# Kernel optimization log

Hardware: AMD Instinct MI355X
Metric: run time of the kernel (lower is better)

## Reference

```python
import jax, jax.numpy as jnp
import numpy as np

N_NODES = 100000
IN_F = 512
HID = 256
HEADS = 1
CLASSES = 40
ALPHA = 0.5
EPS = 1e-5


def layer_norm(x, g, b):
    mu = jnp.mean(x, axis=-1, keepdims=True)
    var = jnp.mean(jnp.square(x - mu), axis=-1, keepdims=True)
    return g * (x - mu) / jnp.sqrt(var + EPS) + b


def full_attention_conv(qs, ks, vs):
    # qs, ks, vs: [N, H, D]; global (Frobenius) L2 normalization as in torch.norm(p=2)
    qs = qs / jnp.linalg.norm(qs.reshape(-1))
    ks = ks / jnp.linalg.norm(ks.reshape(-1))
    N = qs.shape[0]
    kvs = jnp.einsum('lhm,lhd->hmd', ks, vs)                  # [H, D, D]
    attention_num = jnp.einsum('nhm,hmd->nhd', qs, kvs) + N * vs
    ks_sum = jnp.sum(ks, axis=0)                              # [H, D]
    attention_normalizer = jnp.einsum('nhm,hm->nh', qs, ks_sum)[..., None] + N
    return attention_num / attention_normalizer               # [N, H, D]


def trans_layer(h, prev, Wq, bq, Wk, bk, Wv, bv, ln_g, ln_b):
    N = h.shape[0]
    q = (h @ Wq + bq).reshape(N, HEADS, HID)
    k = (h @ Wk + bk).reshape(N, HEADS, HID)
    v = (h @ Wv + bv).reshape(N, HEADS, HID)
    attn = full_attention_conv(q, k, v).mean(axis=1)          # [N, HID]
    h = ALPHA * attn + (1.0 - ALPHA) * prev
    return layer_norm(h, ln_g, ln_b)


def setup_inputs() -> dict:
    key = jax.random.key(0)
    ks = jax.random.split(key, 16)
    s_in = 1.0 / np.sqrt(IN_F)
    s_h = 1.0 / np.sqrt(HID)
    d = {
        'x': jax.random.normal(ks[0], (N_NODES, IN_F), jnp.float32),
        'edge_index': jax.random.randint(ks[1], (2, 1600000), 0, N_NODES, jnp.int64),
        'W_in': jax.random.normal(ks[2], (IN_F, HID), jnp.float32) * s_in,
        'b_in': jnp.zeros((HID,), jnp.float32),
        'ln0_g': jnp.ones((HID,), jnp.float32),
        'ln0_b': jnp.zeros((HID,), jnp.float32),
        'Wq0': jax.random.normal(ks[3], (HID, HID * HEADS), jnp.float32) * s_h,
        'bq0': jnp.zeros((HID * HEADS,), jnp.float32),
        'Wk0': jax.random.normal(ks[4], (HID, HID * HEADS), jnp.float32) * s_h,
        'bk0': jnp.zeros((HID * HEADS,), jnp.float32),
        'Wv0': jax.random.normal(ks[5], (HID, HID * HEADS), jnp.float32) * s_h,
        'bv0': jnp.zeros((HID * HEADS,), jnp.float32),
        'ln1_g': jnp.ones((HID,), jnp.float32),
        'ln1_b': jnp.zeros((HID,), jnp.float32),
        'Wq1': jax.random.normal(ks[6], (HID, HID * HEADS), jnp.float32) * s_h,
        'bq1': jnp.zeros((HID * HEADS,), jnp.float32),
        'Wk1': jax.random.normal(ks[7], (HID, HID * HEADS), jnp.float32) * s_h,
        'bk1': jnp.zeros((HID * HEADS,), jnp.float32),
        'Wv1': jax.random.normal(ks[8], (HID, HID * HEADS), jnp.float32) * s_h,
        'bv1': jnp.zeros((HID * HEADS,), jnp.float32),
        'ln2_g': jnp.ones((HID,), jnp.float32),
        'ln2_b': jnp.zeros((HID,), jnp.float32),
        'W_out': jax.random.normal(ks[9], (HID, CLASSES), jnp.float32) * s_h,
        'b_out': jnp.zeros((CLASSES,), jnp.float32),
    }
    return d


def reference(x, edge_index, W_in, b_in, ln0_g, ln0_b,
              Wq0, bq0, Wk0, bk0, Wv0, bv0, ln1_g, ln1_b,
              Wq1, bq1, Wk1, bk1, Wv1, bv1, ln2_g, ln2_b,
              W_out, b_out):
    # SGFormer forward with use_graph=False, eval mode (dropout no-op).
    h = jax.nn.relu(layer_norm(x @ W_in + b_in, ln0_g, ln0_b))
    prev = h
    h = trans_layer(h, prev, Wq0, bq0, Wk0, bk0, Wv0, bv0, ln1_g, ln1_b)
    prev = h
    h = trans_layer(h, prev, Wq1, bq1, Wk1, bk1, Wv1, bv1, ln2_g, ln2_b)
    return h @ W_out + b_out  # [N, CLASSES]
```

## Files before the change

kernel.cpp:

```cpp
#include <hip/hip_runtime.h>


typedef __attribute__((ext_vector_type(8))) short short8;
typedef __attribute__((ext_vector_type(4))) float floatx4;

__device__ __forceinline__ float bf2f(short u) {
    union { unsigned int i; float f; } v;
    v.i = ((unsigned int)(unsigned short)u) << 16;
    return v.f;
}
__device__ __forceinline__ short f2bf(float f) {
    union { float f; unsigned int i; } v; v.f = f;
    unsigned int b = v.i + 0x7fffu + ((v.i >> 16) & 1u);
    return (short)(b >> 16);
}

#define HID 256
#define MROWS 100000
#define EPSLN 1e-5f

__device__ __forceinline__ void stage_a256(const short* __restrict__ A, short* As,
                                           int row0, int wave, int lane)
{
    const int base = wave * 512;
#pragma unroll
    for (int it = 0; it < 8; ++it) {
        int J = base + it * 64 + lane;
        int row = J >> 5, jj = J & 31;
        int c = jj ^ (row & 31);
        int rowg = min(row0 + row, MROWS - 1);
        const short* gp = A + (size_t)rowg * HID + c * 8;
        __builtin_amdgcn_global_load_lds(
            (const __attribute__((address_space(1))) void*)gp,
            (__attribute__((address_space(3))) void*)&As[(size_t)(base + it * 64) * 8],
            16, 0, 0);
    }
}
__device__ __forceinline__ void stage_lin256(const short* __restrict__ A, short* As,
                                             int row0, int wave, int lane)
{
    const int base = wave * 512;
#pragma unroll
    for (int it = 0; it < 8; ++it) {
        int J = base + it * 64 + lane;
        int row = J >> 5, jj = J & 31;
        int rowg = min(row0 + row, MROWS - 1);
        const short* gp = A + (size_t)rowg * HID + jj * 8;
        __builtin_amdgcn_global_load_lds(
            (const __attribute__((address_space(1))) void*)gp,
            (__attribute__((address_space(3))) void*)&As[(size_t)(base + it * 64) * 8],
            16, 0, 0);
    }
}
__device__ __forceinline__ short8 read_a256(const short* As, int m, int ki, int quad, int l15)
{
    int row = m * 16 + l15;
    int phys = (ki * 4 + quad) ^ (row & 31);
    return *(const short8*)&As[((size_t)row * 32 + phys) * 8];
}

__global__ __launch_bounds__(256, 3)
void qkv_kernel(const short* __restrict__ h,
                const short* __restrict__ BTq, const short* __restrict__ BTk,
                const short* __restrict__ BTv,
                const float* __restrict__ bq, const float* __restrict__ bk,
                const float* __restrict__ bv,
                short* __restrict__ qO, short* __restrict__ kO, short* __restrict__ vO,
                float* __restrict__ sqq, float* __restrict__ sqk,
                float* __restrict__ ksum)
{
    __shared__ short As[64 * 256];
    __shared__ short Cb[16 * 264];
    __shared__ float scr;

    const int tid = threadIdx.x, wave = tid >> 6, lane = tid & 63;
    const int quad = lane >> 4, l15 = lane & 15;
    const int row0 = blockIdx.x * 64, nb = wave * 64;

    stage_a256(h, As, row0, wave, lane);
    __syncthreads();

    const short* BTs[3] = {BTq, BTk, BTv};
    short* Cs[3] = {qO, kO, vO};
    const float* bs[3] = {bq, bk, bv};

#pragma unroll
    for (int out = 0; out < 3; ++out) {
        const short* BT = BTs[out];
        short* C = Cs[out];
        const float* bias = bs[out];

        floatx4 acc[4][4];
#pragma unroll
        for (int m = 0; m < 4; m++)
#pragma unroll
            for (int n = 0; n < 4; n++) acc[m][n] = (floatx4)0.0f;

#pragma unroll
        for (int ki = 0; ki < 8; ++ki) {
            short8 a[4];
#pragma unroll
            for (int m = 0; m < 4; ++m) a[m] = read_a256(As, m, ki, quad, l15);
#pragma unroll
            for (int n = 0; n < 4; ++n) {
                short8 b = *(const short8*)(BT + (size_t)(nb + n * 16 + l15) * 256 + ki * 32 + quad * 8);
#pragma unroll
                for (int m = 0; m < 4; ++m)
                    acc[m][n] = __builtin_amdgcn_mfma_f32_16x16x32_bf16(a[m], b, acc[m][n], 0, 0, 0);
            }
        }

        float bn[4];
#pragma unroll
        for (int n = 0; n < 4; n++) bn[n] = bias[nb + n * 16 + l15];

        float ssq = 0.f;
        float csum[4] = {0.f, 0.f, 0.f, 0.f};
#pragma unroll
        for (int m = 0; m < 4; m++)
#pragma unroll
            for (int r = 0; r < 4; r++) {
                int rl = m * 16 + quad * 4 + r;
                bool valid = (row0 + rl) < MROWS;
#pragma unroll
                for (int n = 0; n < 4; n++) {
                    float val = acc[m][n][r] + bn[n];
                    acc[m][n][r] = val;
                    if (valid) {
                        if (out < 2) ssq += val * val;
                        if (out == 1) csum[n] += val;
                    }
                }
            }
        if (out < 2) {
#pragma unroll
            for (int off = 32; off; off >>= 1) ssq += __shfl_down(ssq, off);
            if (tid == 0) scr = 0.f;
            __syncthreads();
            if (lane == 0) atomicAdd(&scr, ssq);
            __syncthreads();
            if (tid == 0) atomicAdd(out == 0 ? sqq : sqk, scr);
        }
        if (out == 1) {
#pragma unroll
            for (int n = 0; n < 4; n++) {
                float cv = csum[n];
                cv += __shfl_xor(cv, 16);
                cv += __shfl_xor(cv, 32);
                if (quad == 0) atomicAdd(&ksum[nb + n * 16 + l15], cv);
            }
        }
#pragma unroll
        for (int m = 0; m < 4; ++m) {
            __syncthreads();
#pragma unroll
            for (int n = 0; n < 4; ++n)
#pragma unroll
                for (int r = 0; r < 4; ++r)
                    Cb[(quad * 4 + r) * 264 + nb + n * 16 + l15] = f2bf(acc[m][n][r]);
            __syncthreads();
#pragma unroll
            for (int ch = tid; ch < 512; ch += 256) {
                int rl = ch >> 5, co = (ch & 31) * 8;
                int row = row0 + m * 16 + rl;
                if (row < MROWS)
                    *(short8*)(C + (size_t)row * 256 + co) = *(const short8*)&Cb[rl * 264 + co];
            }
        }
    }
}

__global__ __launch_bounds__(256, 3)
void attn_kernel(const short* __restrict__ q, const short* __restrict__ KVt,
                 const short* __restrict__ v, short* __restrict__ h,
                 const float* __restrict__ lng, const float* __restrict__ lnb,
                 float Nf)
{
    __shared__ short As[64 * 256];
    __shared__ short Cb[16 * 264];
    __shared__ float redS[64][4], redQ[64][4];
    __shared__ float rowm[64], rowr[64], denA[64];

    const int tid = threadIdx.x, wave = tid >> 6, lane = tid & 63;
    const int quad = lane >> 4, l15 = lane & 15;
    const int row0 = blockIdx.x * 64, nb = wave * 64;

    stage_a256(q, As, row0, wave, lane);
    __syncthreads();

    floatx4 acc[4][4];
#pragma unroll
    for (int m = 0; m < 4; m++)
#pragma unroll
        for (int n = 0; n < 4; n++) acc[m][n] = (floatx4)0.0f;
    floatx4 accd[4];
#pragma unroll
    for (int m = 0; m < 4; m++) accd[m] = (floatx4)0.0f;

#pragma unroll
    for (int ki = 0; ki < 8; ++ki) {
        short8 a[4];
#pragma unroll
        for (int m = 0; m < 4; ++m) a[m] = read_a256(As, m, ki, quad, l15);
#pragma unroll
        for (int n = 0; n < 4; ++n) {
            short8 b = *(const short8*)(KVt + (size_t)(nb + n * 16 + l15) * 256 + ki * 32 + quad * 8);
#pragma unroll
            for (int m = 0; m < 4; ++m)
                acc[m][n] = __builtin_amdgcn_mfma_f32_16x16x32_bf16(a[m], b, acc[m][n], 0, 0, 0);
        }
        if (wave == 0) {
            short8 bd = *(const short8*)(KVt + (size_t)(256 + l15) * 256 + ki * 32 + quad * 8);
#pragma unroll
            for (int m = 0; m < 4; ++m)
                accd[m] = __builtin_amdgcn_mfma_f32_16x16x32_bf16(a[m], bd, accd[m], 0, 0, 0);
        }
    }
    if (wave == 0 && l15 == 0) {
#pragma unroll
        for (int m = 0; m < 4; m++)
#pragma unroll
            for (int r = 0; r < 4; r++)
                denA[m * 16 + quad * 4 + r] = accd[m][r];
    }
    __syncthreads();

    stage_lin256(v, As, row0, wave, lane);
    __syncthreads();
#pragma unroll
    for (int m = 0; m < 4; m++)
#pragma unroll
        for (int r = 0; r < 4; r++) {
            int rl = m * 16 + quad * 4 + r;
            float rden = 1.0f / (denA[rl] + Nf);
#pragma unroll
            for (int n = 0; n < 4; n++) {
                int col = nb + n * 16 + l15;
                float vv = bf2f(As[(size_t)rl * 256 + col]);
                acc[m][n][r] = 0.5f * (acc[m][n][r] + Nf * vv) * rden;
            }
        }
    __syncthreads();

    stage_lin256(h, As, row0, wave, lane);
    __syncthreads();
#pragma unroll
    for (int m = 0; m < 4; m++)
#pragma unroll
        for (int r = 0; r < 4; r++) {
            int rl = m * 16 + quad * 4 + r;
            float s = 0.f, s2 = 0.f;
#pragma unroll
            for (int n = 0; n < 4; n++) {
                int col = nb + n * 16 + l15;
                float pv = bf2f(As[(size_t)rl * 256 + col]);
                float val = acc[m][n][r] + 0.5f * pv;
                acc[m][n][r] = val;
                s += val; s2 += val * val;
            }
#pragma unroll
            for (int off = 1; off < 16; off <<= 1) {
                s += __shfl_xor(s, off);
                s2 += __shfl_xor(s2, off);
            }
            if (l15 == 0) { redS[rl][wave] = s; redQ[rl][wave] = s2; }
        }
    __syncthreads();
    if (tid < 64) {
        float s = redS[tid][0] + redS[tid][1] + redS[tid][2] + redS[tid][3];
        float s2 = redQ[tid][0] + redQ[tid][1] + redQ[tid][2] + redQ[tid][3];
        float mean = s * (1.0f / 256.0f);
        float var = s2 * (1.0f / 256.0f) - mean * mean;
        rowm[tid] = mean;
        rowr[tid] = rsqrtf(var + EPSLN);
    }
    __syncthreads();
    float g[4], bb[4];
#pragma unroll
    for (int n = 0; n < 4; n++) {
        g[n] = lng[nb + n * 16 + l15];
        bb[n] = lnb[nb + n * 16 + l15];
    }
#pragma unroll
    for (int m = 0; m < 4; ++m) {
        __syncthreads();
#pragma unroll
        for (int n = 0; n < 4; ++n)
#pragma unroll
            for (int r = 0; r < 4; ++r) {
                int rl = m * 16 + quad * 4 + r;
                float x = (acc[m][n][r] - rowm[rl]) * rowr[rl] * g[n] + bb[n];
                Cb[(quad * 4 + r) * 264 + nb + n * 16 + l15] = f2bf(x);
            }
        __syncthreads();
#pragma unroll
        for (int ch = tid; ch < 512; ch += 256) {
            int rl = ch >> 5, co = (ch & 31) * 8;
            int row = row0 + m * 16 + rl;
            if (row < MROWS)
                *(short8*)(h + (size_t)row * 256 + co) = *(const short8*)&Cb[rl * 264 + co];
        }
    }
}

__global__ __launch_bounds__(256, 3)
void in_kernel(const float* __restrict__ x, const short* __restrict__ WinT,
               const float* __restrict__ b_in, const float* __restrict__ lng,
               const float* __restrict__ lnb, short* __restrict__ h)
{
    __shared__ short As[2][64 * 128];
    __shared__ short Cb[16 * 264];
    __shared__ float redS[64][4], redQ[64][4];
    __shared__ float rowm[64], rowr[64];

    const int tid = threadIdx.x, wave = tid >> 6, lane = tid & 63;
    const int quad = lane >> 4, l15 = lane & 15;
    const int row0 = blockIdx.x * 64, nb = wave * 64;

    floatx4 acc[4][4];
#pragma unroll
    for (int m = 0; m < 4; m++)
#pragma unroll
        for (int n = 0; n < 4; n++) acc[m][n] = (floatx4)0.0f;

    floatx4 xr[4][2];
    auto issue = [&](int slab) {
#pragma unroll
        for (int it = 0; it < 4; ++it) {
            int J = it * 256 + tid;
            int row = J >> 4, jj = J & 15, c = jj ^ (row & 15);
            int rowg = min(row0 + row, MROWS - 1);
            const float* gp = x + (size_t)rowg * 512 + slab + c * 8;
            xr[it][0] = *(const floatx4*)gp;
            xr[it][1] = *(const floatx4*)(gp + 4);
        }
    };
    auto commit = [&](short* dst) {
#pragma unroll
        for (int it = 0; it < 4; ++it) {
            int J = it * 256 + tid;
            short8 s8;
#pragma unroll
            for (int i = 0; i < 4; ++i) { s8[i] = f2bf(xr[it][0][i]); s8[i + 4] = f2bf(xr[it][1][i]); }
            *(short8*)&dst[(size_t)J * 8] = s8;
        }
    };

    issue(0);
    commit(As[0]);
    __syncthreads();

#pragma unroll
    for (int s = 0; s < 4; ++s) {
        if (s < 3) issue((s + 1) * 128);
        const short* cur = As[s & 1];
#pragma unroll
        for (int ki = 0; ki < 4; ++ki) {
            short8 a[4];
#pragma unroll
            for (int m = 0; m < 4; ++m) {
                int row = m * 16 + l15;
                int phys = (ki * 4 + quad) ^ (row & 15);
                a[m] = *(const short8*)&cur[((size_t)row * 16 + phys) * 8];
            }
#pragma unroll
            for (int n = 0; n < 4; ++n) {
                short8 b = *(const short8*)(WinT + (size_t)(nb + n * 16 + l15) * 512 + s * 128 + ki * 32 + quad * 8);
#pragma unroll
                for (int m = 0; m < 4; ++m)
                    acc[m][n] = __builtin_amdgcn_mfma_f32_16x16x32_bf16(a[m], b, acc[m][n], 0, 0, 0);
            }
        }
        if (s < 3) {
            commit(As[(s + 1) & 1]);
            __syncthreads();
        }
    }
    float bn[4];
#pragma unroll
    for (int n = 0; n < 4; n++) bn[n] = b_in[nb + n * 16 + l15];
#pragma unroll
    for (int m = 0; m < 4; m++)
#pragma unroll
        for (int r = 0; r < 4; r++) {
            int rl = m * 16 + quad * 4 + r;
            float s = 0.f, s2 = 0.f;
#pragma unroll
            for (int n = 0; n < 4; n++) {
                float val = acc[m][n][r] + bn[n];
                acc[m][n][r] = val;
                s += val; s2 += val * val;
            }
#pragma unroll
            for (int off = 1; off < 16; off <<= 1) {
                s += __shfl_xor(s, off);
                s2 += __shfl_xor(s2, off);
            }
            if (l15 == 0) { redS[rl][wave] = s; redQ[rl][wave] = s2; }
        }
    __syncthreads();
    if (tid < 64) {
        float s = redS[tid][0] + redS[tid][1] + redS[tid][2] + redS[tid][3];
        float s2 = redQ[tid][0] + redQ[tid][1] + redQ[tid][2] + redQ[tid][3];
        float mean = s * (1.0f / 256.0f);
        float var = s2 * (1.0f / 256.0f) - mean * mean;
        rowm[tid] = mean;
        rowr[tid] = rsqrtf(var + EPSLN);
    }
    __syncthreads();
    float g[4], bb[4];
#pragma unroll
    for (int n = 0; n < 4; n++) {
        g[n] = lng[nb + n * 16 + l15];
        bb[n] = lnb[nb + n * 16 + l15];
    }
#pragma unroll
    for (int m = 0; m < 4; ++m) {
        __syncthreads();
#pragma unroll
        for (int n = 0; n < 4; ++n)
#pragma unroll
            for (int r = 0; r < 4; ++r) {
                int rl = m * 16 + quad * 4 + r;
                float xv = (acc[m][n][r] - rowm[rl]) * rowr[rl] * g[n] + bb[n];
                Cb[(quad * 4 + r) * 264 + nb + n * 16 + l15] = f2bf(fmaxf(xv, 0.f));
            }
        __syncthreads();
#pragma unroll
        for (int ch = tid; ch < 512; ch += 256) {
            int rl = ch >> 5, co = (ch & 31) * 8;
            int row = row0 + m * 16 + rl;
            if (row < MROWS)
                *(short8*)(h + (size_t)row * 256 + co) = *(const short8*)&Cb[rl * 264 + co];
        }
    }
}

__global__ __launch_bounds__(256)
void kv_kernel(const short* __restrict__ k, const short* __restrict__ v,
               float* __restrict__ KV, int M)
{
    __shared__ short ksT[128][40];
    __shared__ short vsT[128][40];
    const int t = threadIdx.x, wave = t >> 6, lane = t & 63;
    const int quad = lane >> 4, l15 = lane & 15;
    const int mb = blockIdx.x * 128, nbb = blockIdx.y * 128;
    const int chunk = (M + (int)gridDim.z - 1) / (int)gridDim.z;
    const int rbeg = blockIdx.z * chunk;
    const int rend = min(M, rbeg + chunk);

    floatx4 acc[2][8];
#pragma unroll
    for (int m = 0; m < 2; m++)
#pragma unroll
        for (int j = 0; j < 8; j++) acc[m][j] = (floatx4)0.0f;

    const int lr = t >> 3, c0 = (t & 7) * 16;
    const int wm = wave * 32;

    short8 k0, k1, v0, v1;
    auto loadrow = [&](int gr, short8& a0, short8& a1, short8& b0, short8& b1) {
        a0 = a1 = b0 = b1 = (short8)(short)0;
        if (gr < rend) {
            const short* kp = k + (size_t)gr * HID + mb + c0;
            const short* vp = v + (size_t)gr * HID + nbb + c0;
            a0 = *(const short8*)kp;  a1 = *(const short8*)(kp + 8);
            b0 = *(const short8*)vp;  b1 = *(const short8*)(vp + 8);
        }
    };
    loadrow(rbeg + lr, k0, k1, v0, v1);

    for (int r0 = rbeg; r0 < rend; r0 += 32) {
        __syncthreads();
#pragma unroll
        for (int i = 0; i < 8; i++) {
            ksT[c0 + i][lr] = k0[i];  ksT[c0 + 8 + i][lr] = k1[i];
            vsT[c0 + i][lr] = v0[i];  vsT[c0 + 8 + i][lr] = v1[i];
        }
        __syncthreads();
        bool more = (r0 + 32) < rend;
        short8 nk0, nk1, nv0, nv1;
        if (more) loadrow(r0 + 32 + lr, nk0, nk1, nv0, nv1);
        short8 a0 = *(const short8*)&ksT[wm + l15][quad * 8];
        short8 a1 = *(const short8*)&ksT[wm + 16 + l15][quad * 8];
#pragma unroll
        for (int j = 0; j < 8; j++) {
            short8 b = *(const short8*)&vsT[j * 16 + l15][quad * 8];
            acc[0][j] = __builtin_amdgcn_mfma_f32_16x16x32_bf16(a0, b, acc[0][j], 0, 0, 0);
            acc[1][j] = __builtin_amdgcn_mfma_f32_16x16x32_bf16(a1, b, acc[1][j], 0, 0, 0);
        }
        if (more) { k0 = nk0; k1 = nk1; v0 = nv0; v1 = nv1; }
    }
#pragma unroll
    for (int mi = 0; mi < 2; mi++)
#pragma unroll
        for (int j = 0; j < 8; j++)
#pragma unroll
            for (int r = 0; r < 4; r++) {
                int m = mb + wm + mi * 16 + quad * 4 + r;
                int n = nbb + j * 16 + l15;
                atomicAdd(&KV[(size_t)m * HID + n], acc[mi][j][r]);
            }
}

__global__ void scale_kernel(const float* __restrict__ KV, const float* __restrict__ ksum,
                             const float* __restrict__ sq, short* __restrict__ KVt)
{
    float s = rsqrtf(sq[0]) * rsqrtf(sq[1]);
    int d = blockIdx.x;
    int m = threadIdx.x;
    float val;
    if (d < 256)       val = KV[(size_t)m * HID + d] * s;
    else if (d == 256) val = ksum[m] * s;
    else               val = 0.f;
    KVt[(size_t)d * HID + m] = f2bf(val);
}

__global__ __launch_bounds__(256)
void gemm_out(const short* __restrict__ A, const short* __restrict__ BT,
              const float* __restrict__ bias, float* __restrict__ Out, int M)
{
    const int tid = threadIdx.x, wave = tid >> 6, lane = tid & 63;
    const int quad = lane >> 4, l15 = lane & 15;
    const int row0 = blockIdx.x * 128 + wave * 32;
    const int K = 256;
    floatx4 acc[2][3];
#pragma unroll
    for (int m = 0; m < 2; m++)
#pragma unroll
        for (int n = 0; n < 3; n++) acc[m][n] = (floatx4)0.0f;

    int ra0 = min(row0 + l15, M - 1);
    int ra1 = min(row0 + 16 + l15, M - 1);
    for (int kk = 0; kk < K; kk += 32) {
        short8 a0 = *(const short8*)(A + (size_t)ra0 * K + kk + quad * 8);
        short8 a1 = *(const short8*)(A + (size_t)ra1 * K + kk + quad * 8);
#pragma unroll
        for (int n = 0; n < 3; n++) {
            int col = n * 16 + l15;
            short8 b = (short8)(short)0;
            if (col < 40) b = *(const short8*)(BT + (size_t)col * K + kk + quad * 8);
            acc[0][n] = __builtin_amdgcn_mfma_f32_16x16x32_bf16(a0, b, acc[0][n], 0, 0, 0);
            acc[1][n] = __builtin_amdgcn_mfma_f32_16x16x32_bf16(a1, b, acc[1][n], 0, 0, 0);
        }
    }
#pragma unroll
    for (int m = 0; m < 2; m++)
#pragma unroll
        for (int n = 0; n < 3; n++)
#pragma unroll
            for (int r = 0; r < 4; r++) {
                int row = row0 + m * 16 + quad * 4 + r;
                int col = n * 16 + l15;
                if (row < M && col < 40)
                    Out[(size_t)row * 40 + col] = acc[m][n][r] + bias[col];
            }
}

struct TJobs { const float* src[8]; short* dst[8]; int R[8]; int C[8]; };

__global__ void wtrans(TJobs j)
{
    int job = blockIdx.y;
    int R = j.R[job], Cc = j.C[job];
    const float* s = j.src[job];
    short* d = j.dst[job];
    int n = R * Cc;
    for (int idx = blockIdx.x * 256 + threadIdx.x; idx < n; idx += gridDim.x * 256) {
        int r = idx / Cc, c = idx - r * Cc;
        d[(size_t)c * R + r] = f2bf(s[idx]);
    }
}

__global__ void zerof(float* p, int n)
{
    int i = blockIdx.x * 256 + threadIdx.x;
    if (i < n) p[i] = 0.f;
}

extern "C" void kernel_launch(void* const* d_in, const int* in_sizes, int n_in,
                              void* d_out, int out_size, void* d_ws, size_t ws_size,
                              hipStream_t stream)
{
    const float* x    = (const float*)d_in[0];
    const float* W_in = (const float*)d_in[2];
    const float* b_in = (const float*)d_in[3];
    const float* ln0g = (const float*)d_in[4];
    const float* ln0b = (const float*)d_in[5];
    const float* Wq0  = (const float*)d_in[6];  const float* bq0 = (const float*)d_in[7];
    const float* Wk0  = (const float*)d_in[8];  const float* bk0 = (const float*)d_in[9];
    const float* Wv0  = (const float*)d_in[10]; const float* bv0 = (const float*)d_in[11];
    const float* ln1g = (const float*)d_in[12]; const float* ln1b = (const float*)d_in[13];
    const float* Wq1  = (const float*)d_in[14]; const float* bq1 = (const float*)d_in[15];
    const float* Wk1  = (const float*)d_in[16]; const float* bk1 = (const float*)d_in[17];
    const float* Wv1  = (const float*)d_in[18]; const float* bv1 = (const float*)d_in[19];
    const float* ln2g = (const float*)d_in[20]; const float* ln2b = (const float*)d_in[21];
    const float* W_out = (const float*)d_in[22]; const float* b_out = (const float*)d_in[23];

    const int M = MROWS;
    char* ws = (char*)d_ws;
    size_t off = 0;
    auto alloc = [&](size_t bytes) -> char* {
        char* p = ws + off;
        off += (bytes + 255) & ~(size_t)255;
        return p;
    };
    short* h = (short*)alloc((size_t)M * HID * 2);
    short* q = (short*)alloc((size_t)M * HID * 2);
    short* k = (short*)alloc((size_t)M * HID * 2);
    short* v = (short*)alloc((size_t)M * HID * 2);
    short* WinT  = (short*)alloc((size_t)512 * 256 * 2);
    short* WqT0  = (short*)alloc((size_t)65536 * 2);
    short* WkT0  = (short*)alloc((size_t)65536 * 2);
    short* WvT0  = (short*)alloc((size_t)65536 * 2);
    short* WqT1  = (short*)alloc((size_t)65536 * 2);
    short* WkT1  = (short*)alloc((size_t)65536 * 2);
    short* WvT1  = (short*)alloc((size_t)65536 * 2);
    short* WoutT = (short*)alloc((size_t)40 * 256 * 2);
    float* zbase = (float*)alloc((size_t)(65536 * 2 + 256 * 2 + 4) * 4);
    float* KV0 = zbase;
    float* KV1 = zbase + 65536;
    float* ksum0 = zbase + 131072;
    float* ksum1 = ksum0 + 256;
    float* sq = ksum1 + 256;
    short* KVt0 = (short*)alloc((size_t)272 * 256 * 2);
    short* KVt1 = (short*)alloc((size_t)272 * 256 * 2);

    const int ZN = 65536 * 2 + 256 * 2 + 4;
    zerof<<<dim3((ZN + 255) / 256), 256, 0, stream>>>(zbase, ZN);

    TJobs tj;
    tj.src[0] = W_in;  tj.dst[0] = WinT;  tj.R[0] = 512; tj.C[0] = 256;
    tj.src[1] = Wq0;   tj.dst[1] = WqT0;  tj.R[1] = 256; tj.C[1] = 256;
    tj.src[2] = Wk0;   tj.dst[2] = WkT0;  tj.R[2] = 256; tj.C[2] = 256;
    tj.src[3] = Wv0;   tj.dst[3] = WvT0;  tj.R[3] = 256; tj.C[3] = 256;
    tj.src[4] = Wq1;   tj.dst[4] = WqT1;  tj.R[4] = 256; tj.C[4] = 256;
    tj.src[5] = Wk1;   tj.dst[5] = WkT1;  tj.R[5] = 256; tj.C[5] = 256;
    tj.src[6] = Wv1;   tj.dst[6] = WvT1;  tj.R[6] = 256; tj.C[6] = 256;
    tj.src[7] = W_out; tj.dst[7] = WoutT; tj.R[7] = 256; tj.C[7] = 40;
    wtrans<<<dim3(512, 8), 256, 0, stream>>>(tj);

    const int GB = (M + 63) / 64;
    const float Nf = (float)M;

    in_kernel<<<GB, 256, 0, stream>>>(x, WinT, b_in, ln0g, ln0b, h);
    qkv_kernel<<<GB, 256, 0, stream>>>(h, WqT0, WkT0, WvT0, bq0, bk0, bv0,
                                       q, k, v, sq + 0, sq + 1, ksum0);
    kv_kernel<<<dim3(2, 2, 256), 256, 0, stream>>>(k, v, KV0, M);
    scale_kernel<<<272, 256, 0, stream>>>(KV0, ksum0, sq + 0, KVt0);
    attn_kernel<<<GB, 256, 0, stream>>>(q, KVt0, v, h, ln1g, ln1b, Nf);
    qkv_kernel<<<GB, 256, 0, stream>>>(h, WqT1, WkT1, WvT1, bq1, bk1, bv1,
                                       q, k, v, sq + 2, sq + 3, ksum1);
    kv_kernel<<<dim3(2, 2, 256), 256, 0, stream>>>(k, v, KV1, M);
    scale_kernel<<<272, 256, 0, stream>>>(KV1, ksum1, sq + 2, KVt1);
    attn_kernel<<<GB, 256, 0, stream>>>(q, KVt1, v, h, ln2g, ln2b, Nf);
    gemm_out<<<(M + 127) / 128, 256, 0, stream>>>(h, WoutT, b_out, (float*)d_out, M);
}
```

Before: 1.058 ms.

## Store K and V in MFMA fragment layout and prefetch B operands

The qkv kernel now writes K and V straight from accumulator registers in a per-block MFMA fragment order instead of staging them through shared memory into row-major output. The kv and attention kernels read that fragment layout directly, so attention no longer stages V through LDS. B-operand loads are double-buffered in registers in the GEMM loops, the block-wide atomic reduction is replaced by per-wave atomics, and the launch-bounds occupancy target rises from 3 to 4. The aim is to cut LDS round-trips and barriers. The risks are register pressure at higher occupancy and a tight coupling between the kernels through the custom layout.

```diff
diff --git a/kernel.cpp b/kernel.cpp
--- a/kernel.cpp
+++ b/kernel.cpp
@@ -2,6 +2,7 @@
 
 
 typedef __attribute__((ext_vector_type(8))) short short8;
+typedef __attribute__((ext_vector_type(4))) short short4v;
 typedef __attribute__((ext_vector_type(4))) float floatx4;
 
 __device__ __forceinline__ float bf2f(short u) {
@@ -17,7 +18,12 @@
 
 #define HID 256
 #define MROWS 100000
+#define GBLK 1563
 #define EPSLN 1e-5f
+
+__device__ __forceinline__ size_t fragoff(int blk, int w, int m, int n, int lane) {
+    return (((((size_t)blk * 4 + w) * 4 + m) * 4 + n) * 64 + lane);
+}
 
 __device__ __forceinline__ void stage_a256(const short* __restrict__ A, short* As,
                                            int row0, int wave, int lane)
@@ -59,61 +65,66 @@
     return *(const short8*)&As[((size_t)row * 32 + phys) * 8];
 }
 
-__global__ __launch_bounds__(256, 3)
+__global__ __launch_bounds__(256, 4)
 void qkv_kernel(const short* __restrict__ h,
                 const short* __restrict__ BTq, const short* __restrict__ BTk,
                 const short* __restrict__ BTv,
                 const float* __restrict__ bq, const float* __restrict__ bk,
                 const float* __restrict__ bv,
-                short* __restrict__ qO, short* __restrict__ kO, short* __restrict__ vO,
+                short* __restrict__ qO, short* __restrict__ kF, short* __restrict__ vF,
                 float* __restrict__ sqq, float* __restrict__ sqk,
                 float* __restrict__ ksum)
 {
     __shared__ short As[64 * 256];
-    __shared__ short Cb[16 * 264];
-    __shared__ float scr;
+    __shared__ short Cb[16 * 256];
 
     const int tid = threadIdx.x, wave = tid >> 6, lane = tid & 63;
     const int quad = lane >> 4, l15 = lane & 15;
-    const int row0 = blockIdx.x * 64, nb = wave * 64;
+    const int blk = blockIdx.x;
+    const int row0 = blk * 64, nb = wave * 64;
 
     stage_a256(h, As, row0, wave, lane);
     __syncthreads();
 
-    const short* BTs[3] = {BTq, BTk, BTv};
-    short* Cs[3] = {qO, kO, vO};
-    const float* bs[3] = {bq, bk, bv};
-
-#pragma unroll
-    for (int out = 0; out < 3; ++out) {
-        const short* BT = BTs[out];
-        short* C = Cs[out];
-        const float* bias = bs[out];
-
-        floatx4 acc[4][4];
+    floatx4 acc[4][4];
+
+    auto bload = [&](const short* __restrict__ BT, int n, int ki) -> short8 {
+        return *(const short8*)(BT + (size_t)(nb + n * 16 + l15) * 256 + ki * 32 + quad * 8);
+    };
+    auto gemm256 = [&](const short* __restrict__ BT) {
 #pragma unroll
         for (int m = 0; m < 4; m++)
 #pragma unroll
             for (int n = 0; n < 4; n++) acc[m][n] = (floatx4)0.0f;
-
+        short8 bc[4];
+#pragma unroll
+        for (int n = 0; n < 4; ++n) bc[n] = bload(BT, n, 0);
 #pragma unroll
         for (int ki = 0; ki < 8; ++ki) {
+            short8 bnx[4];
+            if (ki < 7)
+#pragma unroll
+                for (int n = 0; n < 4; ++n) bnx[n] = bload(BT, n, ki + 1);
             short8 a[4];
 #pragma unroll
             for (int m = 0; m < 4; ++m) a[m] = read_a256(As, m, ki, quad, l15);
 #pragma unroll
-            for (int n = 0; n < 4; ++n) {
-                short8 b = *(const short8*)(BT + (size_t)(nb + n * 16 + l15) * 256 + ki * 32 + quad * 8);
+            for (int n = 0; n < 4; ++n)
 #pragma unroll
                 for (int m = 0; m < 4; ++m)
-                    acc[m][n] = __builtin_amdgcn_mfma_f32_16x16x32_bf16(a[m], b, acc[m][n], 0, 0, 0);
-            }
-        }
-
-        float bn[4];
-#pragma unroll
-        for (int n = 0; n < 4; n++) bn[n] = bias[nb + n * 16 + l15];
-
+                    acc[m][n] = __builtin_amdgcn_mfma_f32_16x16x32_bf16(a[m], bc[n], acc[m][n], 0, 0, 0);
+            if (ki < 7)
+#pragma unroll
+                for (int n = 0; n < 4; ++n) bc[n] = bnx[n];
+        }
+    };
+
+    float bn[4];
+
+    gemm256(BTk);
+#pragma unroll
+    for (int n = 0; n < 4; n++) bn[n] = bk[nb + n * 16 + l15];
+    {
         float ssq = 0.f;
         float csum[4] = {0.f, 0.f, 0.f, 0.f};
 #pragma unroll
@@ -126,64 +137,101 @@
                 for (int n = 0; n < 4; n++) {
                     float val = acc[m][n][r] + bn[n];
                     acc[m][n][r] = val;
-                    if (valid) {
-                        if (out < 2) ssq += val * val;
-                        if (out == 1) csum[n] += val;
-                    }
+                    if (valid) { ssq += val * val; csum[n] += val; }
                 }
             }
-        if (out < 2) {
-#pragma unroll
-            for (int off = 32; off; off >>= 1) ssq += __shfl_down(ssq, off);
-            if (tid == 0) scr = 0.f;
-            __syncthreads();
-            if (lane == 0) atomicAdd(&scr, ssq);
-            __syncthreads();
-            if (tid == 0) atomicAdd(out == 0 ? sqq : sqk, scr);
-        }
-        if (out == 1) {
-#pragma unroll
-            for (int n = 0; n < 4; n++) {
-                float cv = csum[n];
-                cv += __shfl_xor(cv, 16);
-                cv += __shfl_xor(cv, 32);
-                if (quad == 0) atomicAdd(&ksum[nb + n * 16 + l15], cv);
-            }
-        }
-#pragma unroll
-        for (int m = 0; m < 4; ++m) {
-            __syncthreads();
-#pragma unroll
-            for (int n = 0; n < 4; ++n)
-#pragma unroll
-                for (int r = 0; r < 4; ++r)
-                    Cb[(quad * 4 + r) * 264 + nb + n * 16 + l15] = f2bf(acc[m][n][r]);
-            __syncthreads();
-#pragma unroll
-            for (int ch = tid; ch < 512; ch += 256) {
-                int rl = ch >> 5, co = (ch & 31) * 8;
-                int row = row0 + m * 16 + rl;
-                if (row < MROWS)
-                    *(short8*)(C + (size_t)row * 256 + co) = *(const short8*)&Cb[rl * 264 + co];
-            }
-        }
-    }
-}
-
-__global__ __launch_bounds__(256, 3)
+#pragma unroll
+        for (int off = 32; off; off >>= 1) ssq += __shfl_down(ssq, off);
+        if (lane == 0) atomicAdd(sqk, ssq);
+#pragma unroll
+        for (int n = 0; n < 4; n++) {
+            float cv = csum[n];
+            cv += __shfl_xor(cv, 16);
+            cv += __shfl_xor(cv, 32);
+            if (quad == 0) atomicAdd(&ksum[nb + n * 16 + l15], cv);
+        }
+#pragma unroll
+        for (int m = 0; m < 4; ++m)
+#pragma unroll
+            for (int n = 0; n < 4; ++n) {
+                short4v s4;
+#pragma unroll
+                for (int r = 0; r < 4; ++r) s4[r] = f2bf(acc[m][n][r]);
+                *(short4v*)(kF + fragoff(blk, wave, m, n, lane) * 4) = s4;
+            }
+    }
+
+    gemm256(BTv);
+#pragma unroll
+    for (int n = 0; n < 4; n++) bn[n] = bv[nb + n * 16 + l15];
+#pragma unroll
+    for (int m = 0; m < 4; ++m)
+#pragma unroll
+        for (int n = 0; n < 4; ++n) {
+            short4v s4;
+#pragma unroll
+            for (int r = 0; r < 4; ++r) s4[r] = f2bf(acc[m][n][r] + bn[n]);
+            *(short4v*)(vF + fragoff(blk, wave, m, n, lane) * 4) = s4;
+        }
+
+    gemm256(BTq);
+#pragma unroll
+    for (int n = 0; n < 4; n++) bn[n] = bq[nb + n * 16 + l15];
+    {
+        float ssq = 0.f;
+#pragma unroll
+        for (int m = 0; m < 4; m++)
+#pragma unroll
+            for (int r = 0; r < 4; r++) {
+                int rl = m * 16 + quad * 4 + r;
+                bool valid = (row0 + rl) < MROWS;
+#pragma unroll
+                for (int n = 0; n < 4; n++) {
+                    float val = acc[m][n][r] + bn[n];
+                    acc[m][n][r] = val;
+                    if (valid) ssq += val * val;
+                }
+            }
+#pragma unroll
+        for (int off = 32; off; off >>= 1) ssq += __shfl_down(ssq, off);
+        if (lane == 0) atomicAdd(sqq, ssq);
+    }
+#pragma unroll
+    for (int m = 0; m < 4; ++m) {
+        __syncthreads();
+#pragma unroll
+        for (int n = 0; n < 4; ++n)
+#pragma unroll
+            for (int r = 0; r < 4; ++r)
+                Cb[(quad * 4 + r) * 256 + nb + n * 16 + l15] = f2bf(acc[m][n][r]);
+        __syncthreads();
+#pragma unroll
+        for (int ch = tid; ch < 512; ch += 256) {
+            int rl = ch >> 5, co = (ch & 31) * 8;
+            int row = row0 + m * 16 + rl;
+            if (row < MROWS)
+                *(short8*)(qO + (size_t)row * 256 + co) = *(const short8*)&Cb[rl * 256 + co];
+        }
+    }
+}
+
+__global__ __launch_bounds__(256, 4)
 void attn_kernel(const short* __restrict__ q, const short* __restrict__ KVt,
-                 const short* __restrict__ v, short* __restrict__ h,
+                 const short* __restrict__ vF, short* __restrict__ h,
                  const float* __restrict__ lng, const float* __restrict__ lnb,
                  float Nf)
 {
     __shared__ short As[64 * 256];
-    __shared__ short Cb[16 * 264];
+    __shared__ float denA[64];
     __shared__ float redS[64][4], redQ[64][4];
-    __shared__ float rowm[64], rowr[64], denA[64];
+    short* Cb = As;
+    float* rowm = (float*)&As[4352];
+    float* rowr = (float*)&As[4480];
 
     const int tid = threadIdx.x, wave = tid >> 6, lane = tid & 63;
     const int quad = lane >> 4, l15 = lane & 15;
-    const int row0 = blockIdx.x * 64, nb = wave * 64;
+    const int blk = blockIdx.x;
+    const int row0 = blk * 64, nb = wave * 64;
 
     stage_a256(q, As, row0, wave, lane);
     __syncthreads();
@@ -216,6 +264,13 @@
                 accd[m] = __builtin_amdgcn_mfma_f32_16x16x32_bf16(a[m], bd, accd[m], 0, 0, 0);
         }
     }
+    short4v vr[4][4];
+#pragma unroll
+    for (int m = 0; m < 4; ++m)
+#pragma unroll
+        for (int n = 0; n < 4; ++n)
+            vr[m][n] = *(const short4v*)(vF + fragoff(blk, wave, m, n, lane) * 4);
+
     if (wave == 0 && l15 == 0) {
 #pragma unroll
         for (int m = 0; m < 4; m++)
@@ -225,8 +280,8 @@
     }
     __syncthreads();
 
-    stage_lin256(v, As, row0, wave, lane);
-    __syncthreads();
+    stage_lin256(h, As, row0, wave, lane);
+
 #pragma unroll
     for (int m = 0; m < 4; m++)
 #pragma unroll
@@ -234,16 +289,11 @@
             int rl = m * 16 + quad * 4 + r;
             float rden = 1.0f / (denA[rl] + Nf);
 #pragma unroll
-            for (int n = 0; n < 4; n++) {
-                int col = nb + n * 16 + l15;
-                float vv = bf2f(As[(size_t)rl * 256 + col]);
-                acc[m][n][r] = 0.5f * (acc[m][n][r] + Nf * vv) * rden;
-            }
+            for (int n = 0; n < 4; n++)
+                acc[m][n][r] = 0.5f * (acc[m][n][r] + Nf * bf2f(vr[m][n][r])) * rden;
         }
     __syncthreads();
 
-    stage_lin256(h, As, row0, wave, lane);
-    __syncthreads();
 #pragma unroll
     for (int m = 0; m < 4; m++)
 #pragma unroll
@@ -274,7 +324,6 @@
         rowm[tid] = mean;
         rowr[tid] = rsqrtf(var + EPSLN);
     }
-    __syncthreads();
     float g[4], bb[4];
 #pragma unroll
     for (int n = 0; n < 4; n++) {
@@ -290,7 +339,7 @@
             for (int r = 0; r < 4; ++r) {
                 int rl = m * 16 + quad * 4 + r;
                 float x = (acc[m][n][r] - rowm[rl]) * rowr[rl] * g[n] + bb[n];
-                Cb[(quad * 4 + r) * 264 + nb + n * 16 + l15] = f2bf(x);
+                Cb[(quad * 4 + r) * 256 + nb + n * 16 + l15] = f2bf(x);
             }
         __syncthreads();
 #pragma unroll
@@ -298,7 +347,7 @@
             int rl = ch >> 5, co = (ch & 31) * 8;
             int row = row0 + m * 16 + rl;
             if (row < MROWS)
-                *(short8*)(h + (size_t)row * 256 + co) = *(const short8*)&Cb[rl * 264 + co];
+                *(short8*)(h + (size_t)row * 256 + co) = *(const short8*)&Cb[rl * 256 + co];
         }
     }
 }
@@ -345,6 +394,9 @@
             *(short8*)&dst[(size_t)J * 8] = s8;
         }
     };
+    auto bload = [&](int s, int ki, int n) -> short8 {
+        return *(const short8*)(WinT + (size_t)(nb + n * 16 + l15) * 512 + s * 128 + ki * 32 + quad * 8);
+    };
 
     issue(0);
     commit(As[0]);
@@ -354,8 +406,15 @@
     for (int s = 0; s < 4; ++s) {
         if (s < 3) issue((s + 1) * 128);
         const short* cur = As[s & 1];
+        short8 bc[4];
+#pragma unroll
+        for (int n = 0; n < 4; ++n) bc[n] = bload(s, 0, n);
 #pragma unroll
         for (int ki = 0; ki < 4; ++ki) {
+            short8 bnx[4];
+            if (ki < 3)
+#pragma unroll
+                for (int n = 0; n < 4; ++n) bnx[n] = bload(s, ki + 1, n);
             short8 a[4];
 #pragma unroll
             for (int m = 0; m < 4; ++m) {
@@ -364,12 +423,13 @@
                 a[m] = *(const short8*)&cur[((size_t)row * 16 + phys) * 8];
             }
 #pragma unroll
-            for (int n = 0; n < 4; ++n) {
-                short8 b = *(const short8*)(WinT + (size_t)(nb + n * 16 + l15) * 512 + s * 128 + ki * 32 + quad * 8);
+            for (int n = 0; n < 4; ++n)
 #pragma unroll
                 for (int m = 0; m < 4; ++m)
-                    acc[m][n] = __builtin_amdgcn_mfma_f32_16x16x32_bf16(a[m], b, acc[m][n], 0, 0, 0);
-            }
+                    acc[m][n] = __builtin_amdgcn_mfma_f32_16x16x32_bf16(a[m], bc[n], acc[m][n], 0, 0, 0);
+            if (ki < 3)
+#pragma unroll
+                for (int n = 0; n < 4; ++n) bc[n] = bnx[n];
         }
         if (s < 3) {
             commit(As[(s + 1) & 1]);
@@ -437,7 +497,7 @@
 }
 
 __global__ __launch_bounds__(256)
-void kv_kernel(const short* __restrict__ k, const short* __restrict__ v,
+void kv_kernel(const short* __restrict__ kF, const short* __restrict__ vF,
                float* __restrict__ KV, int M)
 {
     __shared__ short ksT[128][40];
@@ -445,9 +505,8 @@
     const int t = threadIdx.x, wave = t >> 6, lane = t & 63;
     const int quad = lane >> 4, l15 = lane & 15;
     const int mb = blockIdx.x * 128, nbb = blockIdx.y * 128;
-    const int chunk = (M + (int)gridDim.z - 1) / (int)gridDim.z;
-    const int rbeg = blockIdx.z * chunk;
-    const int rend = min(M, rbeg + chunk);
+    const int bbeg = blockIdx.z * 7;
+    const int bend = min(GBLK, bbeg + 7);
 
     floatx4 acc[2][8];
 #pragma unroll
@@ -455,42 +514,52 @@
 #pragma unroll
         for (int j = 0; j < 8; j++) acc[m][j] = (floatx4)0.0f;
 
-    const int lr = t >> 3, c0 = (t & 7) * 16;
     const int wm = wave * 32;
 
-    short8 k0, k1, v0, v1;
-    auto loadrow = [&](int gr, short8& a0, short8& a1, short8& b0, short8& b1) {
-        a0 = a1 = b0 = b1 = (short8)(short)0;
-        if (gr < rend) {
-            const short* kp = k + (size_t)gr * HID + mb + c0;
-            const short* vp = v + (size_t)gr * HID + nbb + c0;
-            a0 = *(const short8*)kp;  a1 = *(const short8*)(kp + 8);
-            b0 = *(const short8*)vp;  b1 = *(const short8*)(vp + 8);
+    short4v kc[4], vc[4];
+    auto loadstripe = [&](int blk, int half) {
+#pragma unroll
+        for (int i = 0; i < 4; ++i) {
+            int ci = t + i * 256;
+            int colc = ci & 127, rowg = ci >> 7;
+            int qs = rowg & 3, mi = rowg >> 2;
+            int m = half * 2 + mi;
+            bool valid = (blk * 64 + m * 16 + qs * 4) < M;
+            int Ck = mb + colc, Cv = nbb + colc;
+            size_t ok = fragoff(blk, Ck >> 6, m, (Ck >> 4) & 3, qs * 16 + (Ck & 15)) * 4;
+            size_t ov = fragoff(blk, Cv >> 6, m, (Cv >> 4) & 3, qs * 16 + (Cv & 15)) * 4;
+            kc[i] = valid ? *(const short4v*)(kF + ok) : (short4v)(short)0;
+            vc[i] = valid ? *(const short4v*)(vF + ov) : (short4v)(short)0;
         }
     };
-    loadrow(rbeg + lr, k0, k1, v0, v1);
-
-    for (int r0 = rbeg; r0 < rend; r0 += 32) {
-        __syncthreads();
-#pragma unroll
-        for (int i = 0; i < 8; i++) {
-            ksT[c0 + i][lr] = k0[i];  ksT[c0 + 8 + i][lr] = k1[i];
-            vsT[c0 + i][lr] = v0[i];  vsT[c0 + 8 + i][lr] = v1[i];
-        }
-        __syncthreads();
-        bool more = (r0 + 32) < rend;
-        short8 nk0, nk1, nv0, nv1;
-        if (more) loadrow(r0 + 32 + lr, nk0, nk1, nv0, nv1);
-        short8 a0 = *(const short8*)&ksT[wm + l15][quad * 8];
-        short8 a1 = *(const short8*)&ksT[wm + 16 + l15][quad * 8];
-#pragma unroll
-        for (int j = 0; j < 8; j++) {
-            short8 b = *(const short8*)&vsT[j * 16 + l15][quad * 8];
-            acc[0][j] = __builtin_amdgcn_mfma_f32_16x16x32_bf16(a0, b, acc[0][j], 0, 0, 0);
-            acc[1][j] = __builtin_amdgcn_mfma_f32_16x16x32_bf16(a1, b, acc[1][j], 0, 0, 0);
-        }
-        if (more) { k0 = nk0; k1 = nk1; v0 = nv0; v1 = nv1; }
-    }
+    auto commit = [&]() {
+#pragma unroll
+        for (int i = 0; i < 4; ++i) {
+            int ci = t + i * 256;
+            int colc = ci & 127, rowg = ci >> 7;
+            *(short4v*)&ksT[colc][rowg * 4] = kc[i];
+            *(short4v*)&vsT[colc][rowg * 4] = vc[i];
+        }
+    };
+
+    loadstripe(bbeg, 0);
+    for (int blk = bbeg; blk < bend; ++blk)
+#pragma unroll
+        for (int half = 0; half < 2; ++half) {
+            __syncthreads();
+            commit();
+            __syncthreads();
+            bool more = !(blk == bend - 1 && half == 1);
+            if (more) loadstripe(half ? blk + 1 : blk, half ^ 1);
+            short8 a0 = *(const short8*)&ksT[wm + l15][quad * 8];
+            short8 a1 = *(const short8*)&ksT[wm + 16 + l15][quad * 8];
+#pragma unroll
+            for (int j = 0; j < 8; j++) {
+                short8 b = *(const short8*)&vsT[j * 16 + l15][quad * 8];
+                acc[0][j] = __builtin_amdgcn_mfma_f32_16x16x32_bf16(a0, b, acc[0][j], 0, 0, 0);
+                acc[1][j] = __builtin_amdgcn_mfma_f32_16x16x32_bf16(a1, b, acc[1][j], 0, 0, 0);
+            }
+        }
 #pragma unroll
     for (int mi = 0; mi < 2; mi++)
 #pragma unroll
@@ -598,6 +667,7 @@
     const float* W_out = (const float*)d_in[22]; const float* b_out = (const float*)d_in[23];
 
     const int M = MROWS;
+    const int MPAD = GBLK * 64;
     char* ws = (char*)d_ws;
     size_t off = 0;
     auto alloc = [&](size_t bytes) -> char* {
@@ -607,8 +677,8 @@
     };
     short* h = (short*)alloc((size_t)M * HID * 2);
     short* q = (short*)alloc((size_t)M * HID * 2);
-    short* k = (short*)alloc((size_t)M * HID * 2);
-    short* v = (short*)alloc((size_t)M * HID * 2);
+    short* k = (short*)alloc((size_t)MPAD * HID * 2);
+    short* v = (short*)alloc((size_t)MPAD * HID * 2);
     short* WinT  = (short*)alloc((size_t)512 * 256 * 2);
     short* WqT0  = (short*)alloc((size_t)65536 * 2);
     short* WkT0  = (short*)alloc((size_t)65536 * 2);
@@ -640,18 +710,19 @@
     tj.src[7] = W_out; tj.dst[7] = WoutT; tj.R[7] = 256; tj.C[7] = 40;
     wtrans<<<dim3(512, 8), 256, 0, stream>>>(tj);
 
-    const int GB = (M + 63) / 64;
+    const int GB = GBLK;
     const float Nf = (float)M;
+    const int ZB = (GBLK + 6) / 7;
 
     in_kernel<<<GB, 256, 0, stream>>>(x, WinT, b_in, ln0g, ln0b, h);
     qkv_kernel<<<GB, 256, 0, stream>>>(h, WqT0, WkT0, WvT0, bq0, bk0, bv0,
                                        q, k, v, sq + 0, sq + 1, ksum0);
-    kv_kernel<<<dim3(2, 2, 256), 256, 0, stream>>>(k, v, KV0, M);
+    kv_kernel<<<dim3(2, 2, ZB), 256, 0, stream>>>(k, v, KV0, M);
     scale_kernel<<<272, 256, 0, stream>>>(KV0, ksum0, sq + 0, KVt0);
     attn_kernel<<<GB, 256, 0, stream>>>(q, KVt0, v, h, ln1g, ln1b, Nf);
     qkv_kernel<<<GB, 256, 0, stream>>>(h, WqT1, WkT1, WvT1, bq1, bk1, bv1,
                                        q, k, v, sq + 2, sq + 3, ksum1);
-    kv_kernel<<<dim3(2, 2, 256), 256, 0, stream>>>(k, v, KV1, M);
+    kv_kernel<<<dim3(2, 2, ZB), 256, 0, stream>>>(k, v, KV1, M);
     scale_kernel<<<272, 256, 0, stream>>>(KV1, ksum1, sq + 2, KVt1);
     attn_kernel<<<GB, 256, 0, stream>>>(q, KVt1, v, h, ln2g, ln2b, Nf);
     gemm_out<<<(M + 127) / 128, 256, 0, stream>>>(h, WoutT, b_out, (float*)d_out, M);
```

Measured after the change: 1.273 ms. +20.3%, slower.
